# Optimization experiments

Hardware: AMD Instinct MI355X
Metric: run time of the kernel (lower is better)

## Reference

```python
import jax, jax.numpy as jnp
import numpy as np

B, S, E, A = 64, 1024, 512, 128


def setup_inputs() -> dict:
    key = jax.random.key(0)
    ks = jax.random.split(key, 12)
    sc = 0.02
    states = jax.random.normal(ks[0], (B, S, E), jnp.float32)
    cls_token = jax.random.normal(ks[1], (B, E), jnp.float32)
    # ragged lengths in [2, S]; force at least one full-length row so padded width == S-1
    lengths = jax.random.randint(ks[2], (B,), 2, S + 1).at[0].set(S).astype(jnp.int32)
    position_action = (jax.random.randint(ks[3], (B,), 0, S) % (lengths - 1)).astype(jnp.int32)
    symbol_action = jax.random.randint(ks[4], (B,), 0, A).astype(jnp.int32)
    W1p = jax.random.normal(ks[5], (2 * E, 2 * E), jnp.float32) * sc
    b1p = jnp.zeros((2 * E,), jnp.float32)
    w2p = jax.random.normal(ks[6], (2 * E,), jnp.float32) * sc
    b2p = jnp.zeros((1,), jnp.float32)
    W1s = jax.random.normal(ks[7], (2 * E, 2 * E), jnp.float32) * sc
    b1s = jnp.zeros((2 * E,), jnp.float32)
    W2s = jax.random.normal(ks[8], (2 * E, A), jnp.float32) * sc
    b2s = jnp.zeros((A,), jnp.float32)
    Wc1 = jax.random.normal(ks[9], (E, E), jnp.float32) * sc
    bc1 = jnp.zeros((E,), jnp.float32)
    wc2 = jax.random.normal(ks[10], (E,), jnp.float32) * sc
    bc2 = jnp.zeros((1,), jnp.float32)
    return dict(states=states, cls_token=cls_token, W1p=W1p, b1p=b1p, w2p=w2p, b2p=b2p,
                W1s=W1s, b1s=b1s, W2s=W2s, b2s=b2s, Wc1=Wc1, bc1=bc1, wc2=wc2, bc2=bc2,
                lengths=lengths, position_action=position_action, symbol_action=symbol_action)


def reference(states, cls_token, W1p, b1p, w2p, b2p, W1s, b1s, W2s, b2s,
              Wc1, bc1, wc2, bc2, lengths, position_action, symbol_action):
    b, s, e = states.shape
    # --- get_adjacent_pairs + position_actor MLP, fused (no [.,2E] concat materialized) ---
    first, second = states[:, :-1], states[:, 1:]            # (B, S-1, E) each
    h = jax.nn.relu(jnp.einsum('bse,ef->bsf', first, W1p[:e])
                    + jnp.einsum('bse,ef->bsf', second, W1p[e:]) + b1p)  # (B, S-1, 2E)
    scores = jnp.einsum('bsf,f->bs', h, w2p) + b2p            # (B, S-1)
    # --- map_scores_to_sentences: pad invalid pair slots with -inf ---
    pos_mask = jnp.arange(s - 1)[None, :] < (lengths - 1)[:, None]
    scores = jnp.where(pos_mask, scores, -jnp.inf)
    logp = jax.nn.log_softmax(scores, axis=1)
    logp_pos = jnp.take_along_axis(logp, position_action[:, None], axis=1)[:, 0]
    logp_m = jnp.where(pos_mask, logp, 0.0)                   # safe for -inf slots
    ent_pos = -jnp.sum(jnp.exp(logp) * logp_m, axis=1)
    # --- symbol head on the pair embedding at the chosen split position ---
    bidx = jnp.arange(b)
    e1 = states[bidx, position_action]                        # (B, E)
    e2 = states[bidx, position_action + 1]                    # (B, E)
    sh = jax.nn.relu(e1 @ W1s[:e] + e2 @ W1s[e:] + b1s)       # (B, 2E)
    slogp = jax.nn.log_softmax(sh @ W2s + b2s, axis=1)        # (B, A)
    logp_sym = jnp.take_along_axis(slogp, symbol_action[:, None], axis=1)[:, 0]
    ent_sym = -jnp.sum(jnp.exp(slogp) * slogp, axis=1)
    # --- critic on cls token ---
    val = jax.nn.relu(cls_token @ Wc1 + bc1) @ wc2 + bc2      # (B,)
    return jnp.stack([logp_pos, logp_sym, val, ent_pos, ent_sym], axis=0)  # (5, B)
```

## Files before the change

### kernel.cpp

```cpp
#include <hip/hip_runtime.h>
#include <stdint.h>

#define BDIM 64
#define SDIM 1024
#define EDIM 512
#define ADIM 128
#define M_ROWS (BDIM*(SDIM-1))
#define KDIM 1024
#define NDIM 1024

typedef unsigned short u16;
typedef __attribute__((ext_vector_type(8))) short short8;
typedef __attribute__((ext_vector_type(4))) float floatx4;
typedef const __attribute__((address_space(1))) void as1_void;
typedef __attribute__((address_space(3))) void as3_void;

__device__ inline u16 f2bf(float f){
  unsigned int u = __float_as_uint(f);
  u += 0x7fffu + ((u >> 16) & 1u);
  return (u16)(u >> 16);
}

__global__ __launch_bounds__(1024) void k_prep(
    const float* __restrict__ states, const float* __restrict__ cls,
    const float* __restrict__ W1p, const float* __restrict__ W1s,
    const float* __restrict__ b1s, const float* __restrict__ Wc1,
    const float* __restrict__ bc1, const float* __restrict__ wc2,
    const float* __restrict__ bc2, const int* __restrict__ lengths,
    const int* __restrict__ pos_action,
    u16* __restrict__ sbf, u16* __restrict__ wt,
    float* __restrict__ sh, int* __restrict__ rows, int* __restrict__ aux,
    float* __restrict__ scores, float* __restrict__ out)
{
  __shared__ float smem[64*65];
  const int blk = blockIdx.x, tid = threadIdx.x;

  if (blk < 1024){
    int i = blk*1024 + tid;
#pragma unroll
    for (int it = 0; it < 4; ++it, i += 1048576){
      int row = i >> 6;
      int s = row & 1023, b = row >> 10;
      if (s < lengths[b]){
        const float4* sp = (const float4*)states + (size_t)i*2;
        float4 a = sp[0], c = sp[1];
        short8 v;
        v[0]=(short)f2bf(a.x); v[1]=(short)f2bf(a.y); v[2]=(short)f2bf(a.z); v[3]=(short)f2bf(a.w);
        v[4]=(short)f2bf(c.x); v[5]=(short)f2bf(c.y); v[6]=(short)f2bf(c.z); v[7]=(short)f2bf(c.w);
        ((short8*)sbf)[i] = v;
      }
    }
    return;
  }
  if (blk < 1280){
    float (*tile)[65] = (float(*)[65])smem;
    int tb = blk - 1024;
    int zi = tb*1024 + tid;
    if (zi < 65536) scores[zi] = 0.f;
    int k0 = (tb & 15)*64, n0 = (tb >> 4)*64;
    int tx = tid & 63, ty = tid >> 6;
    for (int j = ty; j < 64; j += 16) tile[j][tx] = W1p[(size_t)(k0+j)*NDIM + n0 + tx];
    __syncthreads();
    for (int j = ty; j < 64; j += 16) wt[(size_t)(n0+j)*KDIM + k0 + tx] = f2bf(tile[tx][j]);
    return;
  }
  if (blk == 1280){
    __shared__ int scum[65];
    if (tid == 0){
      int c = 0;
      for (int b = 0; b < 64; ++b){ scum[b] = c; c += lengths[b] - 1; }
      scum[64] = c;
    }
    __syncthreads();
    if (tid < 65) aux[tid] = scum[tid];
    if (tid == 0){
      aux[70] = scum[64];
      aux[71] = (scum[64] + 127) >> 7;
    }
    for (int b = 0; b < 64; ++b){
      int base = scum[b], L = scum[b+1] - scum[b];
      for (int i2 = tid; i2 < L; i2 += 1024) rows[base + i2] = (b << 10) + i2;
    }
    return;
  }
  if (blk < 1537){
    float* xs  = smem;
    float* red = smem + 1024;
    int rb = blk - 1281;
    int b = rb >> 2, n0 = (rb & 3)*256;
    int pa = pos_action[b];
    const float* src = states + (size_t)(b*SDIM + pa) * EDIM;
    xs[tid] = src[tid];
    __syncthreads();
    int n = n0 + (tid & 255);
    int k0 = (tid >> 8) * 256;
    float acc = 0.f;
#pragma unroll 8
    for (int jj = 0; jj < 256; ++jj){
      int k = k0 + jj;
      acc = fmaf(xs[k], W1s[(size_t)k*1024 + n], acc);
    }
    red[tid] = acc;
    __syncthreads();
    if (tid < 256){
      float s = red[tid] + red[tid+256] + red[tid+512] + red[tid+768];
      sh[b*1024 + n0 + tid] = fmaxf(s + b1s[n0 + tid], 0.f);
    }
    return;
  }
  {
    float* xs  = smem;
    float* red = smem + 512;
    float* r2  = smem + 1536;
    int b = blk - 1537;
    if (tid < 512) xs[tid] = cls[b*EDIM + tid];
    __syncthreads();
    int n = tid & 511;
    int k0 = (tid >> 9) * 256;
    float acc = 0.f;
#pragma unroll 8
    for (int jj = 0; jj < 256; ++jj){
      int k = k0 + jj;
      acc = fmaf(xs[k], Wc1[(size_t)k*EDIM + n], acc);
    }
    red[tid] = acc;
    __syncthreads();
    float p = 0.f;
    if (tid < 512){
      float h = red[tid] + red[tid + 512];
      p = fmaxf(h + bc1[tid], 0.f) * wc2[tid];
    }
    for (int off = 32; off; off >>= 1) p += __shfl_xor(p, off);
    if ((tid & 63) == 0) r2[tid >> 6] = p;
    __syncthreads();
    if (tid == 0){
      float s = bc2[0];
#pragma unroll
      for (int jj = 0; jj < 16; ++jj) s += r2[jj];
      out[128 + b] = s;
    }
  }
}

__global__ __launch_bounds__(256, 2) void k_gemm_scores(
    const u16* __restrict__ sbf, const u16* __restrict__ wt,
    const float* __restrict__ b1p, const float* __restrict__ w2p,
    const int* __restrict__ rows, const int* __restrict__ aux,
    float* __restrict__ scores)
{
  __shared__ short8 Ash[1024];
  __shared__ short8 Bsh[1024];
  const int tid = threadIdx.x;
  const int w = tid >> 6, l = tid & 63;
  const int j = blockIdx.x;
  const int tl = ((j >> 6) << 3) | (j & 7);
  const int nt = (j >> 3) & 7;
  const int total = aux[70];
  if (tl >= aux[71]) return;

  const int lrow8 = l >> 3;
  const int c = (l & 7) ^ lrow8;
  const char* sbase = (const char*)sbf;
  const char* wbase = (const char*)wt;
  int offA[4], offB[4];
#pragma unroll
  for (int i = 0; i < 4; ++i){
    int mloc = (w*4 + i)*8 + lrow8;
    int mg = tl*128 + mloc;
    if (mg >= total) mg = 0;
    int rs = rows[mg];
    offA[i] = rs*1024 + c*16;
    int nloc = (w*4 + i)*8 + lrow8;
    offB[i] = (nt*128 + nloc)*2048 + c*16;
  }

  const int r = l & 15, q = l >> 4;
  const int wm = w & 1, wn = w >> 1;
  int aIdx[4], bIdx[4];
#pragma unroll
  for (int i = 0; i < 4; ++i){
    int m = wm*64 + i*16 + r;
    aIdx[i] = m*8 + (q ^ (r & 7));
    int n = wn*64 + i*16 + r;
    bIdx[i] = n*8 + (q ^ (r & 7));
  }

  floatx4 acc[4][4];
#pragma unroll
  for (int a = 0; a < 4; ++a)
#pragma unroll
    for (int b = 0; b < 4; ++b) acc[a][b] = (floatx4)(0.0f);

  for (int step = 0; step < 16; ++step){
    const int ktb = step * 128;
    __syncthreads();
#pragma unroll
    for (int i = 0; i < 4; ++i){
      __builtin_amdgcn_global_load_lds((as1_void*)(sbase + offA[i] + ktb),
                                       (as3_void*)((char*)Ash + (w*4 + i)*1024), 16, 0, 0);
    }
#pragma unroll
    for (int i = 0; i < 4; ++i){
      __builtin_amdgcn_global_load_lds((as1_void*)(wbase + offB[i] + ktb),
                                       (as3_void*)((char*)Bsh + (w*4 + i)*1024), 16, 0, 0);
    }
    __syncthreads();
#pragma unroll
    for (int kh = 0; kh < 2; ++kh){
      short8 af[4], bf[4];
#pragma unroll
      for (int i = 0; i < 4; ++i) af[i] = Ash[aIdx[i] ^ (kh*4)];
#pragma unroll
      for (int i = 0; i < 4; ++i) bf[i] = Bsh[bIdx[i] ^ (kh*4)];
#pragma unroll
      for (int mi = 0; mi < 4; ++mi)
#pragma unroll
        for (int ni = 0; ni < 4; ++ni)
          acc[mi][ni] = __builtin_amdgcn_mfma_f32_16x16x32_bf16(af[mi], bf[ni], acc[mi][ni], 0, 0, 0);
    }
  }

  const int mrow0 = tl*128 + wm*64;
  const int ncol0 = nt*128 + wn*64;
#pragma unroll
  for (int mi = 0; mi < 4; ++mi){
    float t0 = 0.f, t1 = 0.f, t2 = 0.f, t3 = 0.f;
#pragma unroll
    for (int ni = 0; ni < 4; ++ni){
      int n = ncol0 + ni*16 + r;
      float bb = b1p[n], ww = w2p[n];
      floatx4 a = acc[mi][ni];
      t0 += fmaxf(a[0] + bb, 0.f) * ww;
      t1 += fmaxf(a[1] + bb, 0.f) * ww;
      t2 += fmaxf(a[2] + bb, 0.f) * ww;
      t3 += fmaxf(a[3] + bb, 0.f) * ww;
    }
#pragma unroll
    for (int off = 1; off < 16; off <<= 1){
      t0 += __shfl_xor(t0, off);
      t1 += __shfl_xor(t1, off);
      t2 += __shfl_xor(t2, off);
      t3 += __shfl_xor(t3, off);
    }
    if (r == 0){
      int row = mrow0 + mi*16 + q*4;
      if (row + 0 < total) atomicAdd(&scores[row + 0], t0);
      if (row + 1 < total) atomicAdd(&scores[row + 1], t1);
      if (row + 2 < total) atomicAdd(&scores[row + 2], t2);
      if (row + 3 < total) atomicAdd(&scores[row + 3], t3);
    }
  }
}

__global__ __launch_bounds__(1024) void k_post(
    const float* __restrict__ scores, const float* __restrict__ sh,
    const float* __restrict__ W2s, const float* __restrict__ b2s,
    const int* __restrict__ aux, const int* __restrict__ lengths,
    const int* __restrict__ pos_action, const int* __restrict__ sym_action,
    float* __restrict__ out)
{
  __shared__ float smem[2208];
  const int blk = blockIdx.x, tid = threadIdx.x;
  if (blk < 64){
    float* sc   = smem;
    float* red  = smem + 1024;
    float* red2 = smem + 1040;
    int b = blk;
    int L = lengths[b] - 1;
    const float* sp = scores + aux[b];
    float mx = -1e30f;
    for (int s = tid; s < L; s += 1024){
      float v = sp[s];
      sc[s] = v;
      mx = fmaxf(mx, v);
    }
    for (int off = 32; off; off >>= 1) mx = fmaxf(mx, __shfl_xor(mx, off));
    if ((tid & 63) == 0) red[tid >> 6] = mx;
    __syncthreads();
    mx = -1e30f;
#pragma unroll
    for (int jj = 0; jj < 16; ++jj) mx = fmaxf(mx, red[jj]);
    float se = 0.f, ses = 0.f;
    for (int s = tid; s < L; s += 1024){
      float v = sc[s];
      float e = expf(v - mx);
      se += e; ses += e * v;
    }
    for (int off = 32; off; off >>= 1){ se += __shfl_xor(se, off); ses += __shfl_xor(ses, off); }
    __syncthreads();
    if ((tid & 63) == 0){ red[tid >> 6] = se; red2[tid >> 6] = ses; }
    __syncthreads();
    if (tid == 0){
      float S = 0.f, SS = 0.f;
#pragma unroll
      for (int jj = 0; jj < 16; ++jj){ S += red[jj]; SS += red2[jj]; }
      float logZ = logf(S);
      int pa = pos_action[b];
      out[b]       = sc[pa] - mx - logZ;
      out[192 + b] = mx + logZ - SS / S;
    }
    return;
  }
  {
    float* xs  = smem;
    float* red = smem + 1024;
    float* lg  = smem + 2048;
    float* r2  = smem + 2176;
    float* r3  = smem + 2192;
    int b = blk - 64;
    xs[tid] = sh[b*1024 + tid];
    __syncthreads();
    int n = tid & 127;
    int f0 = (tid >> 7) * 128;
    float acc = 0.f;
#pragma unroll 8
    for (int jj = 0; jj < 128; ++jj){
      int f = f0 + jj;
      acc = fmaf(xs[f], W2s[(size_t)f*ADIM + n], acc);
    }
    red[tid] = acc;
    __syncthreads();
    if (tid < 128){
      float s = b2s[tid];
#pragma unroll
      for (int jj = 0; jj < 8; ++jj) s += red[tid + jj*128];
      lg[tid] = s;
    }
    __syncthreads();
    float v = (tid < 128) ? lg[tid] : -1e30f;
    float mx = v;
    for (int off = 32; off; off >>= 1) mx = fmaxf(mx, __shfl_xor(mx, off));
    if ((tid & 63) == 0) r2[tid >> 6] = mx;
    __syncthreads();
    mx = -1e30f;
#pragma unroll
    for (int jj = 0; jj < 16; ++jj) mx = fmaxf(mx, r2[jj]);
    float e = (tid < 128) ? expf(v - mx) : 0.f;
    float se = e, ses = (tid < 128) ? e * v : 0.f;
    for (int off = 32; off; off >>= 1){ se += __shfl_xor(se, off); ses += __shfl_xor(ses, off); }
    __syncthreads();
    if ((tid & 63) == 0){ r2[tid >> 6] = se; r3[tid >> 6] = ses; }
    __syncthreads();
    if (tid == 0){
      float S = 0.f, SS = 0.f;
#pragma unroll
      for (int jj = 0; jj < 16; ++jj){ S += r2[jj]; SS += r3[jj]; }
      float logZ = logf(S);
      out[64 + b]  = lg[sym_action[b]] - mx - logZ;
      out[256 + b] = mx + logZ - SS / S;
    }
  }
}

extern "C" void kernel_launch(void* const* d_in, const int* in_sizes, int n_in,
                              void* d_out, int out_size, void* d_ws, size_t ws_size,
                              hipStream_t stream){
  const float* states = (const float*)d_in[0];
  const float* cls    = (const float*)d_in[1];
  const float* W1p    = (const float*)d_in[2];
  const float* b1p    = (const float*)d_in[3];
  const float* w2p    = (const float*)d_in[4];
  const float* W1s    = (const float*)d_in[6];
  const float* b1s    = (const float*)d_in[7];
  const float* W2s    = (const float*)d_in[8];
  const float* b2s    = (const float*)d_in[9];
  const float* Wc1    = (const float*)d_in[10];
  const float* bc1    = (const float*)d_in[11];
  const float* wc2    = (const float*)d_in[12];
  const float* bc2    = (const float*)d_in[13];
  const int* lengths  = (const int*)d_in[14];
  const int* pos_a    = (const int*)d_in[15];
  const int* sym_a    = (const int*)d_in[16];
  float* out = (float*)d_out;

  char* ws = (char*)d_ws;
  u16* sbf      = (u16*)ws;
  u16* wt       = (u16*)(ws + 67108864);
  float* scores = (float*)(ws + 69206016);
  float* sh     = (float*)(ws + 69468160);
  int* rows     = (int*)(ws + 69730304);
  int* aux      = (int*)(ws + 69992448);

  k_prep<<<1601, 1024, 0, stream>>>(states, cls, W1p, W1s, b1s, Wc1, bc1, wc2, bc2,
                                    lengths, pos_a, sbf, wt, sh, rows, aux, scores, out);
  k_gemm_scores<<<4096, 256, 0, stream>>>(sbf, wt, b1p, w2p, rows, aux, scores);
  k_post<<<128, 1024, 0, stream>>>(scores, sh, W2s, b2s, aux, lengths, pos_a, sym_a, out);
}
```

Measured before the change: 323.1 us.

## Enlarge GEMM tile to 256x256 with double-buffered LDS prefetch pipeline

The scores GEMM moves from 128x128 tiles with 256 threads to 256x256 tiles with 512 threads (8 waves). It uses a 128KB double-buffered LDS ring, staging the next k-step in half-tile chunks interleaved with MFMA phases, with explicit vmcnt/lgkmcnt waits, sched barriers and s_setprio. The goal is to overlap global-to-LDS loads with matrix math and raise operand reuse per byte loaded. In exchange it adds register pressure from 32 accumulators per thread, uses more LDS per block which lowers occupancy, and makes the hand-written waitcnt schedule easy to get subtly wrong.

```diff
diff --git a/kernel.cpp b/kernel.cpp
--- a/kernel.cpp
+++ b/kernel.cpp
@@ -5,7 +5,6 @@
 #define SDIM 1024
 #define EDIM 512
 #define ADIM 128
-#define M_ROWS (BDIM*(SDIM-1))
 #define KDIM 1024
 #define NDIM 1024
 
@@ -76,6 +75,7 @@
     if (tid == 0){
       aux[70] = scum[64];
       aux[71] = (scum[64] + 127) >> 7;
+      aux[72] = (scum[64] + 255) >> 8;
     }
     for (int b = 0; b < 64; ++b){
       int base = scum[b], L = scum[b+1] - scum[b];
@@ -142,88 +142,147 @@
   }
 }
 
-__global__ __launch_bounds__(256, 2) void k_gemm_scores(
+__global__ __launch_bounds__(512, 2) void k_gemm_scores(
     const u16* __restrict__ sbf, const u16* __restrict__ wt,
     const float* __restrict__ b1p, const float* __restrict__ w2p,
     const int* __restrict__ rows, const int* __restrict__ aux,
     float* __restrict__ scores)
 {
-  __shared__ short8 Ash[1024];
-  __shared__ short8 Bsh[1024];
+  __shared__ short8 L[8192];
   const int tid = threadIdx.x;
   const int w = tid >> 6, l = tid & 63;
   const int j = blockIdx.x;
-  const int tl = ((j >> 6) << 3) | (j & 7);
-  const int nt = (j >> 3) & 7;
+  const int tl = ((j >> 5) << 3) | (j & 7);
+  const int nt = (j >> 3) & 3;
   const int total = aux[70];
-  if (tl >= aux[71]) return;
-
-  const int lrow8 = l >> 3;
-  const int c = (l & 7) ^ lrow8;
-  const char* sbase = (const char*)sbf;
-  const char* wbase = (const char*)wt;
-  int offA[4], offB[4];
-#pragma unroll
-  for (int i = 0; i < 4; ++i){
-    int mloc = (w*4 + i)*8 + lrow8;
-    int mg = tl*128 + mloc;
-    if (mg >= total) mg = 0;
-    int rs = rows[mg];
-    offA[i] = rs*1024 + c*16;
-    int nloc = (w*4 + i)*8 + lrow8;
-    offB[i] = (nt*128 + nloc)*2048 + c*16;
-  }
+  if (tl >= aux[72]) return;
+
+  const int swzc = ((tid & 3) ^ ((tid >> 4) & 3)) * 16;
+  unsigned int srcA0, srcA1, srcB0, srcB1;
+  {
+    int rl0 = (tid >> 2), rl1 = 128 + (tid >> 2);
+    int mg0 = tl*256 + rl0; if (mg0 >= total) mg0 = 0;
+    int mg1 = tl*256 + rl1; if (mg1 >= total) mg1 = 0;
+    srcA0 = (unsigned)rows[mg0]*1024u + (unsigned)swzc;
+    srcA1 = (unsigned)rows[mg1]*1024u + (unsigned)swzc;
+    srcB0 = (unsigned)(nt*256 + rl0)*2048u + (unsigned)swzc;
+    srcB1 = (unsigned)(nt*256 + rl1)*2048u + (unsigned)swzc;
+  }
+  const char* sb = (const char*)sbf;
+  const char* wb = (const char*)wt;
+  char* Lb = (char*)L;
+  const int ldsw = w*1024;
+
+#define STG(ga, lo) __builtin_amdgcn_global_load_lds((as1_void*)(ga), (as3_void*)(Lb + (lo)), 16, 0, 0)
+#define STAGE_A(kt, kh, slot) do{ unsigned go = (unsigned)(kt)*128u + (unsigned)(kh)*64u; \
+    STG(sb + srcA0 + go, (slot)*65536 + (kh)*16384 +        ldsw); \
+    STG(sb + srcA1 + go, (slot)*65536 + (kh)*16384 + 8192 + ldsw); }while(0)
+#define STAGE_B(kt, kh, slot) do{ unsigned go = (unsigned)(kt)*128u + (unsigned)(kh)*64u; \
+    STG(wb + srcB0 + go, (slot)*65536 + 32768 + (kh)*16384 +        ldsw); \
+    STG(wb + srcB1 + go, (slot)*65536 + 32768 + (kh)*16384 + 8192 + ldsw); }while(0)
+#define BARRIER __builtin_amdgcn_s_barrier()
+#define LGKM0 do{ asm volatile("s_waitcnt lgkmcnt(0)" ::: "memory"); __builtin_amdgcn_sched_barrier(0); }while(0)
+#define VM4 do{ __builtin_amdgcn_sched_barrier(0); asm volatile("s_waitcnt vmcnt(4)" ::: "memory"); }while(0)
 
   const int r = l & 15, q = l >> 4;
   const int wm = w & 1, wn = w >> 1;
-  int aIdx[4], bIdx[4];
-#pragma unroll
-  for (int i = 0; i < 4; ++i){
-    int m = wm*64 + i*16 + r;
-    aIdx[i] = m*8 + (q ^ (r & 7));
-    int n = wn*64 + i*16 + r;
-    bIdx[i] = n*8 + (q ^ (r & 7));
-  }
-
-  floatx4 acc[4][4];
-#pragma unroll
-  for (int a = 0; a < 4; ++a)
+  const int fsw = q ^ ((r >> 2) & 3);
+  const int aB = (wm*128 + r)*4 + fsw;
+  const int bB = 2048 + (wn*64 + r)*4 + fsw;
+
+  floatx4 acc[8][4];
+#pragma unroll
+  for (int a = 0; a < 8; ++a)
 #pragma unroll
     for (int b = 0; b < 4; ++b) acc[a][b] = (floatx4)(0.0f);
 
-  for (int step = 0; step < 16; ++step){
-    const int ktb = step * 128;
-    __syncthreads();
-#pragma unroll
-    for (int i = 0; i < 4; ++i){
-      __builtin_amdgcn_global_load_lds((as1_void*)(sbase + offA[i] + ktb),
-                                       (as3_void*)((char*)Ash + (w*4 + i)*1024), 16, 0, 0);
-    }
-#pragma unroll
-    for (int i = 0; i < 4; ++i){
-      __builtin_amdgcn_global_load_lds((as1_void*)(wbase + offB[i] + ktb),
-                                       (as3_void*)((char*)Bsh + (w*4 + i)*1024), 16, 0, 0);
-    }
-    __syncthreads();
-#pragma unroll
-    for (int kh = 0; kh < 2; ++kh){
-      short8 af[4], bf[4];
-#pragma unroll
-      for (int i = 0; i < 4; ++i) af[i] = Ash[aIdx[i] ^ (kh*4)];
-#pragma unroll
-      for (int i = 0; i < 4; ++i) bf[i] = Bsh[bIdx[i] ^ (kh*4)];
-#pragma unroll
-      for (int mi = 0; mi < 4; ++mi)
-#pragma unroll
-        for (int ni = 0; ni < 4; ++ni)
-          acc[mi][ni] = __builtin_amdgcn_mfma_f32_16x16x32_bf16(af[mi], bf[ni], acc[mi][ni], 0, 0, 0);
-    }
-  }
-
-  const int mrow0 = tl*128 + wm*64;
-  const int ncol0 = nt*128 + wn*64;
-#pragma unroll
-  for (int mi = 0; mi < 4; ++mi){
+  STAGE_A(0,0,0); STAGE_B(0,0,0);
+  STAGE_A(0,1,0); STAGE_B(0,1,0);
+  STAGE_A(1,0,1); STAGE_B(1,0,1);
+  __builtin_amdgcn_sched_barrier(0);
+  asm volatile("s_waitcnt vmcnt(4)" ::: "memory");
+  BARRIER;
+
+  short8 af[4], bf[4];
+#pragma unroll 2
+  for (int t = 0; t < 16; ++t){
+    const int s  = t & 1;
+    const int so = s ^ 1;
+    const int sb16 = s*4096;
+    const int kt1 = (t+1) & 15, kt2 = (t+2) & 15;
+
+#pragma unroll
+    for (int i = 0; i < 4; ++i) af[i] = L[sb16 + aB + i*64];
+#pragma unroll
+    for (int i = 0; i < 4; ++i) bf[i] = L[sb16 + bB + i*64];
+    STAGE_A(kt1, 1, so);
+    BARRIER; LGKM0;
+    __builtin_amdgcn_s_setprio(1);
+#pragma unroll
+    for (int mi = 0; mi < 4; ++mi)
+#pragma unroll
+      for (int ni = 0; ni < 4; ++ni)
+        acc[mi][ni] = __builtin_amdgcn_mfma_f32_16x16x32_bf16(af[mi], bf[ni], acc[mi][ni], 0, 0, 0);
+    __builtin_amdgcn_s_setprio(0);
+    BARRIER;
+
+#pragma unroll
+    for (int i = 0; i < 4; ++i) af[i] = L[sb16 + aB + (4+i)*64];
+    STAGE_B(kt1, 1, so);
+    BARRIER; LGKM0;
+    __builtin_amdgcn_s_setprio(1);
+#pragma unroll
+    for (int mi = 0; mi < 4; ++mi)
+#pragma unroll
+      for (int ni = 0; ni < 4; ++ni)
+        acc[4+mi][ni] = __builtin_amdgcn_mfma_f32_16x16x32_bf16(af[mi], bf[ni], acc[4+mi][ni], 0, 0, 0);
+    __builtin_amdgcn_s_setprio(0);
+    VM4;
+    BARRIER;
+
+#pragma unroll
+    for (int i = 0; i < 4; ++i) af[i] = L[sb16 + 1024 + aB + i*64];
+#pragma unroll
+    for (int i = 0; i < 4; ++i) bf[i] = L[sb16 + 1024 + bB + i*64];
+    STAGE_A(kt2, 0, s);
+    BARRIER; LGKM0;
+    __builtin_amdgcn_s_setprio(1);
+#pragma unroll
+    for (int mi = 0; mi < 4; ++mi)
+#pragma unroll
+      for (int ni = 0; ni < 4; ++ni)
+        acc[mi][ni] = __builtin_amdgcn_mfma_f32_16x16x32_bf16(af[mi], bf[ni], acc[mi][ni], 0, 0, 0);
+    __builtin_amdgcn_s_setprio(0);
+    BARRIER;
+
+#pragma unroll
+    for (int i = 0; i < 4; ++i) af[i] = L[sb16 + 1024 + aB + (4+i)*64];
+    STAGE_B(kt2, 0, s);
+    BARRIER; LGKM0;
+    __builtin_amdgcn_s_setprio(1);
+#pragma unroll
+    for (int mi = 0; mi < 4; ++mi)
+#pragma unroll
+      for (int ni = 0; ni < 4; ++ni)
+        acc[4+mi][ni] = __builtin_amdgcn_mfma_f32_16x16x32_bf16(af[mi], bf[ni], acc[4+mi][ni], 0, 0, 0);
+    __builtin_amdgcn_s_setprio(0);
+    VM4;
+    BARRIER;
+  }
+  __builtin_amdgcn_sched_barrier(0);
+  asm volatile("s_waitcnt vmcnt(0)" ::: "memory");
+
+#undef STG
+#undef STAGE_A
+#undef STAGE_B
+#undef BARRIER
+#undef LGKM0
+#undef VM4
+
+  const int mrow0 = tl*256 + wm*128;
+  const int ncol0 = nt*256 + wn*64;
+#pragma unroll
+  for (int mi = 0; mi < 8; ++mi){
     float t0 = 0.f, t1 = 0.f, t2 = 0.f, t3 = 0.f;
 #pragma unroll
     for (int ni = 0; ni < 4; ++ni){
@@ -383,6 +442,6 @@
 
   k_prep<<<1601, 1024, 0, stream>>>(states, cls, W1p, W1s, b1s, Wc1, bc1, wc2, bc2,
                                     lengths, pos_a, sbf, wt, sh, rows, aux, scores, out);
-  k_gemm_scores<<<4096, 256, 0, stream>>>(sbf, wt, b1p, w2p, rows, aux, scores);
+  k_gemm_scores<<<1024, 512, 0, stream>>>(sbf, wt, b1p, w2p, rows, aux, scores);
   k_post<<<128, 1024, 0, stream>>>(scores, sh, W2s, b2s, aux, lengths, pos_a, sym_a, out);
 }
```

Measured after the change: 347.2 us. +7.4%, slower.
